# Kernel optimization log

Hardware: AMD Instinct MI355X
Metric: run time of the kernel (lower is better)

The kernel has to match this reference:

```python
import jax, jax.numpy as jnp
import numpy as np

THRESHOLD = 0.0  # default float threshold, non-learned path
SURROGATE_TAU = 0.1

@jax.custom_vjp
def jumprelu(x):
    # Forward: hard threshold x * 1[x > THRESHOLD]
    return x * (x > THRESHOLD).astype(x.dtype)

def _jumprelu_fwd(x):
    return jumprelu(x), x

def _jumprelu_bwd(x, g):
    # Smooth surrogate gradient of x * sigmoid(x/tau)
    tau = SURROGATE_TAU
    sig = jax.nn.sigmoid(x / tau)
    surrogate = sig + x * sig * (1.0 - sig) / tau
    return (g * surrogate,)

jumprelu.defvjp(_jumprelu_fwd, _jumprelu_bwd)

NUM_TRANSFORMS = 64
D_MODEL = 2048
RANK = 32
BATCH = 2048

def setup_inputs() -> dict:
    key = jax.random.key(0)
    kx, kv, ku, ke = jax.random.split(key, 4)
    scale = (1.0 / (D_MODEL * RANK)) ** 0.25
    x = jax.random.normal(kx, (BATCH, D_MODEL), dtype=jnp.float32)
    V = jax.random.normal(kv, (NUM_TRANSFORMS, RANK, D_MODEL), dtype=jnp.float32) * scale
    U = jax.random.normal(ku, (NUM_TRANSFORMS, D_MODEL, RANK), dtype=jnp.float32) * scale
    encoder = jax.random.normal(ke, (NUM_TRANSFORMS, D_MODEL), dtype=jnp.float32)
    encoder = encoder / jnp.linalg.norm(encoder, axis=1, keepdims=True)
    bias = jnp.full((NUM_TRANSFORMS,), -1.0, dtype=jnp.float32)
    return {"x": x, "V": V, "U": U, "encoder": encoder, "bias": bias}

def reference(x, V, U, encoder, bias):
    # pre_acts: (batch, num_transforms)
    pre_acts = x @ encoder.T - bias
    gate = jumprelu(pre_acts)
    # Vx: (n, b, r); UVx: (n, b, d)
    Vx = jnp.einsum('nrd,bd->nbr', V, x)
    UVx = jnp.einsum('ndr,nbr->nbd', U, Vx)
    gated = UVx * gate.T[:, :, None]
    output = gated.sum(axis=0)  # (batch, d_model)
    u_norms = jnp.linalg.norm(U.reshape(U.shape[0], -1), axis=1)
    v_norms = jnp.linalg.norm(V.reshape(V.shape[0], -1), axis=1)
    frobenius_norms = u_norms * v_norms / (D_MODEL * RANK) ** 0.5
    return (output, gate, frobenius_norms)
```

## Files before the change

### kernel.cpp

```cpp
#include <hip/hip_runtime.h>


#define D_MODEL 2048
#define BATCH   2048
#define NT      64
#define RANK    32

typedef __attribute__((ext_vector_type(8))) __bf16 bf16x8;
typedef __attribute__((ext_vector_type(4))) float  f32x4;

__device__ __forceinline__ unsigned short f2bf(float f) {
  unsigned int u = __builtin_bit_cast(unsigned int, f);
  u += 0x7FFFu + ((u >> 16) & 1u);
  return (unsigned short)(u >> 16);
}

__device__ __forceinline__ void gload_lds16(const void* g, void* l) {
  __builtin_amdgcn_global_load_lds(
      (const __attribute__((address_space(1))) unsigned int*)g,
      (__attribute__((address_space(3))) unsigned int*)l,
      16, 0, 0);
}


__device__ __forceinline__ void block_reduce_store(float ss, float* dst, int slot) {
  __shared__ float red[256];
  int t = threadIdx.x;
  red[t] = ss;
  __syncthreads();
  for (int s = 128; s > 0; s >>= 1) {
    if (t < s) red[t] += red[t + s];
    __syncthreads();
  }
  if (t == 0) dst[slot] = red[0];
}

__global__ void k_prep(const float4* __restrict__ x, const float4* __restrict__ enc,
                       const float4* __restrict__ V, const float4* __restrict__ U,
                       ushort4* __restrict__ xb, ushort4* __restrict__ encb,
                       ushort4* __restrict__ Vb, unsigned short* __restrict__ Ut,
                       float* __restrict__ partV, float* __restrict__ partU) {
  int bid = blockIdx.x, t = threadIdx.x;
  if (bid < 1024) {
#pragma unroll
    for (int it = 0; it < 4; ++it) {
      int i = bid * 1024 + it * 256 + t;
      float4 v = x[i];
      ushort4 o;
      o.x = f2bf(v.x); o.y = f2bf(v.y); o.z = f2bf(v.z); o.w = f2bf(v.w);
      xb[i] = o;
    }
  } else if (bid < 1152) {
    int i = (bid - 1024) * 256 + t;
    float4 v = enc[i];
    ushort4 o;
    o.x = f2bf(v.x); o.y = f2bf(v.y); o.z = f2bf(v.z); o.w = f2bf(v.w);
    encb[i] = o;
  } else if (bid < 1408) {
    int b = bid - 1152;
    size_t base4 = (size_t)b * 4096;
    float ss = 0.f;
    for (int it = 0; it < 16; ++it) {
      size_t idx = base4 + t + it * 256;
      float4 v = V[idx];
      ss += v.x * v.x + v.y * v.y + v.z * v.z + v.w * v.w;
      ushort4 o;
      o.x = f2bf(v.x); o.y = f2bf(v.y); o.z = f2bf(v.z); o.w = f2bf(v.w);
      Vb[idx] = o;
    }
    block_reduce_store(ss, partV, b);
  } else {
    int b = bid - 1408;
    int n = b >> 2;
    size_t base4 = (size_t)b * 4096;
    float ss = 0.f;
    for (int it = 0; it < 16; ++it) {
      size_t idx4 = base4 + t + it * 256;
      float4 v = U[idx4];
      ss += v.x * v.x + v.y * v.y + v.z * v.z + v.w * v.w;
      size_t e = idx4 * 4 - (size_t)n * (D_MODEL * RANK);
      int dcol = (int)(e >> 5);
      int r = (int)(e & 31);
      ushort4 o;
      o.x = f2bf(v.x); o.y = f2bf(v.y); o.z = f2bf(v.z); o.w = f2bf(v.w);
      *(ushort4*)(Ut + (size_t)dcol * 2048 + n * 32 + r) = o;
    }
    block_reduce_store(ss, partU, b);
  }
}

__global__ void k_gate_reduce(const float* __restrict__ part, const float* __restrict__ bias,
                              float* __restrict__ gate,
                              const float* __restrict__ pU, const float* __restrict__ pV,
                              float* __restrict__ frob) {
  int t = threadIdx.x;
  if (blockIdx.x == 0 && t < NT) {
    float su = pU[4 * t] + pU[4 * t + 1] + pU[4 * t + 2] + pU[4 * t + 3];
    float sv = pV[4 * t] + pV[4 * t + 1] + pV[4 * t + 2] + pV[4 * t + 3];
    frob[t] = sqrtf(su) * sqrtf(sv) * (1.0f / 256.0f);
  }
#pragma unroll
  for (int u = 0; u < 4; ++u) {
    int idx = blockIdx.x * 1024 + u * 256 + t;
    float s = 0.f;
#pragma unroll
    for (int z = 0; z < 8; ++z) s += part[(size_t)z * (BATCH * NT) + idx];
    float pre = s - bias[idx & (NT - 1)];
    gate[idx] = pre > 0.f ? pre : 0.f;
  }
}

template <int WGM, int WGN, int MI, int NJ, int EPI, int SWZ, int TEAMS>
__global__ __launch_bounds__(TEAMS * 256, 4)
void gemm_bt(const unsigned short* __restrict__ A,
             const unsigned short* __restrict__ Bt,
             const float* __restrict__ aux,
             unsigned short* __restrict__ outB,
             float* __restrict__ outF, int K, int klen) {
  constexpr int BM = WGM * MI * 16;
  constexpr int BN = WGN * NJ * 16;
  constexpr int RA = BM / 32;
  constexpr int RB = BN / 32;
  __shared__ __align__(16) unsigned short smem[TEAMS * (BM + BN) * 64];

  const int tid = threadIdx.x;
  const int w = tid >> 6;
  const int lane = tid & 63;
  const int quad = lane >> 4;
  const int l15 = lane & 15;
  const int team = w >> 2;
  const int wl = w & 3;
  const int wm = wl % WGM;
  const int wn = wl / WGM;

  unsigned short* As = smem + team * (BM + BN) * 64;
  unsigned short* Bs = As + BM * 64;

  int blockM, blockN, kbeg;
  if constexpr (SWZ) {
    const int lin = blockIdx.x;
    const int xcd = lin & 7;
    const int i = lin >> 3;
    blockM = (xcd & 1) * 8 + (i & 7);
    blockN = (xcd >> 1) * 8 + (i >> 3);
    kbeg = 0;
  } else {
    blockN = blockIdx.x;
    blockM = blockIdx.y;
    kbeg = blockIdx.z * klen;
  }
  const int kspan = klen / TEAMS;
  kbeg += team * kspan;

  const int lrow = lane >> 3;
  const int lq = (lane & 7) ^ lrow;
  const unsigned short* Ag = A + (size_t)(blockM * BM + lrow) * K + kbeg + lq * 8;
  const unsigned short* Bg = Bt + (size_t)(blockN * BN + lrow) * K + kbeg + lq * 8;

  const int pcs = (quad ^ (lane & 7)) * 16;
  const int rfA = wm * MI * 16 + l15;
  const int rfB = wn * NJ * 16 + l15;

  f32x4 acc[MI][NJ];
  const f32x4 z = {0.f, 0.f, 0.f, 0.f};
#pragma unroll
  for (int i = 0; i < MI; ++i)
#pragma unroll
    for (int j = 0; j < NJ; ++j) acc[i][j] = z;

  for (int k0 = 0; k0 < kspan; k0 += 64) {
#pragma unroll
    for (int j = 0; j < RA; ++j)
      gload_lds16(Ag + (size_t)((j * 4 + wl) * 8) * K + k0,
                  (char*)As + (j * 4 + wl) * 1024);
#pragma unroll
    for (int j = 0; j < RB; ++j)
      gload_lds16(Bg + (size_t)((j * 4 + wl) * 8) * K + k0,
                  (char*)Bs + (j * 4 + wl) * 1024);
    __syncthreads();
#pragma unroll
    for (int s = 0; s < 2; ++s) {
      bf16x8 af[MI], bfr[NJ];
#pragma unroll
      for (int i = 0; i < MI; ++i)
        af[i] = *(const bf16x8*)((const char*)As + (rfA + i * 16) * 128 + (pcs ^ (s << 6)));
#pragma unroll
      for (int j = 0; j < NJ; ++j)
        bfr[j] = *(const bf16x8*)((const char*)Bs + (rfB + j * 16) * 128 + (pcs ^ (s << 6)));
#pragma unroll
      for (int i = 0; i < MI; ++i)
#pragma unroll
        for (int j = 0; j < NJ; ++j)
          acc[i][j] = __builtin_amdgcn_mfma_f32_16x16x32_bf16(af[i], bfr[j], acc[i][j], 0, 0, 0);
    }
    __syncthreads();
  }

  if constexpr (TEAMS == 2) {
    float4* red = (float4*)smem;
    if (team == 1) {
#pragma unroll
      for (int i = 0; i < MI; ++i)
#pragma unroll
        for (int j = 0; j < NJ; ++j) {
          float4 v = {acc[i][j][0], acc[i][j][1], acc[i][j][2], acc[i][j][3]};
          red[((wl * MI + i) * NJ + j) * 64 + lane] = v;
        }
    }
    __syncthreads();
    if (team == 1) return;
#pragma unroll
    for (int i = 0; i < MI; ++i)
#pragma unroll
      for (int j = 0; j < NJ; ++j) {
        float4 r = red[((wl * MI + i) * NJ + j) * 64 + lane];
        acc[i][j][0] += r.x; acc[i][j][1] += r.y;
        acc[i][j][2] += r.z; acc[i][j][3] += r.w;
      }
  }

  const int row0 = blockM * BM + wm * MI * 16 + quad * 4;
  const int col0 = blockN * BN + wn * NJ * 16 + l15;
#pragma unroll
  for (int i = 0; i < MI; ++i) {
#pragma unroll
    for (int j = 0; j < NJ; ++j) {
      const int col = col0 + j * 16;
#pragma unroll
      for (int t = 0; t < 4; ++t) {
        const int row = row0 + i * 16 + t;
        float v = acc[i][j][t];
        if constexpr (EPI == 0) {
          float g = aux[(size_t)row * NT + (col >> 5)];
          outB[(size_t)row * 2048 + col] = f2bf(v * g);
        } else if constexpr (EPI == 1) {
          outF[(size_t)row * 2048 + col] = v;
        } else {
          outF[(size_t)blockIdx.z * (BATCH * NT) + (size_t)row * NT + col] = v;
        }
      }
    }
  }
}


extern "C" void kernel_launch(void* const* d_in, const int* in_sizes, int n_in,
                              void* d_out, int out_size, void* d_ws, size_t ws_size,
                              hipStream_t stream) {
  const float* x    = (const float*)d_in[0];
  const float* V    = (const float*)d_in[1];
  const float* U    = (const float*)d_in[2];
  const float* enc  = (const float*)d_in[3];
  const float* bias = (const float*)d_in[4];

  float* out  = (float*)d_out;
  float* gate = out + (size_t)BATCH * D_MODEL;
  float* frob = gate + (size_t)BATCH * NT;

  char* ws = (char*)d_ws;
  unsigned short* xb   = (unsigned short*)(ws);
  unsigned short* Vb   = (unsigned short*)(ws + (8u << 20));
  unsigned short* Ut   = (unsigned short*)(ws + (16u << 20));
  unsigned short* Yg   = (unsigned short*)(ws + (24u << 20));
  float* gatePart      = (float*)Yg;
  unsigned short* encb = (unsigned short*)(ws + (32u << 20));
  float* partU = (float*)(ws + (32u << 20) + 262144);
  float* partV = partU + 256;

  k_prep<<<1664, 256, 0, stream>>>((const float4*)x, (const float4*)enc,
                                   (const float4*)V, (const float4*)U,
                                   (ushort4*)xb, (ushort4*)encb, (ushort4*)Vb, Ut,
                                   partV, partU);

  gemm_bt<4, 1, 2, 4, 3, 0, 1><<<dim3(1, 16, 8), 256, 0, stream>>>(
      xb, encb, nullptr, nullptr, gatePart, D_MODEL, 256);
  k_gate_reduce<<<128, 256, 0, stream>>>(gatePart, bias, gate, partU, partV, frob);

  gemm_bt<2, 2, 4, 2, 0, 1, 2><<<dim3(512, 1, 1), 512, 0, stream>>>(
      xb, Vb, gate, Yg, nullptr, D_MODEL, D_MODEL);

  gemm_bt<2, 2, 4, 2, 1, 1, 2><<<dim3(512, 1, 1), 512, 0, stream>>>(
      Yg, Ut, nullptr, nullptr, out, D_MODEL, D_MODEL);
}
```

Before: 154.3 us.

## Double-buffer LDS in GEMM and replace split-K teams with larger tiles

Drops the two-team intra-block split-K reduction from the bf16 GEMM kernel. It now double-buffers the LDS tiles so the next K-slice's global-to-LDS loads overlap the current MFMA work, using one barrier per iteration instead of two. The two big GEMMs now use 8 waves per 128x128 tile (256 blocks instead of 512), with a new XCD-aware block swizzle and launch bounds of 2. The trade is more LDS per block and fewer blocks to hide latency, in exchange for removing the LDS reduction and overlapping loads with compute.

```diff
diff --git a/kernel.cpp b/kernel.cpp
--- a/kernel.cpp
+++ b/kernel.cpp
@@ -110,47 +110,42 @@
   }
 }
 
-template <int WGM, int WGN, int MI, int NJ, int EPI, int SWZ, int TEAMS>
-__global__ __launch_bounds__(TEAMS * 256, 4)
+template <int WGM, int WGN, int MI, int NJ, int EPI, int SWZ>
+__global__ __launch_bounds__(WGM * WGN * 64, 2)
 void gemm_bt(const unsigned short* __restrict__ A,
              const unsigned short* __restrict__ Bt,
              const float* __restrict__ aux,
              unsigned short* __restrict__ outB,
              float* __restrict__ outF, int K, int klen) {
+  constexpr int VW = WGM * WGN;
   constexpr int BM = WGM * MI * 16;
   constexpr int BN = WGN * NJ * 16;
-  constexpr int RA = BM / 32;
-  constexpr int RB = BN / 32;
-  __shared__ __align__(16) unsigned short smem[TEAMS * (BM + BN) * 64];
+  constexpr int GA = (BM / 8) / VW;
+  constexpr int GB = (BN / 8) / VW;
+  constexpr int HBUF = (BM + BN) * 64;
+  __shared__ __align__(16) unsigned short smem[2 * HBUF];
 
   const int tid = threadIdx.x;
   const int w = tid >> 6;
   const int lane = tid & 63;
   const int quad = lane >> 4;
   const int l15 = lane & 15;
-  const int team = w >> 2;
-  const int wl = w & 3;
-  const int wm = wl % WGM;
-  const int wn = wl / WGM;
-
-  unsigned short* As = smem + team * (BM + BN) * 64;
-  unsigned short* Bs = As + BM * 64;
+  const int wm = w % WGM;
+  const int wn = w / WGM;
 
   int blockM, blockN, kbeg;
   if constexpr (SWZ) {
     const int lin = blockIdx.x;
     const int xcd = lin & 7;
     const int i = lin >> 3;
-    blockM = (xcd & 1) * 8 + (i & 7);
-    blockN = (xcd >> 1) * 8 + (i >> 3);
+    blockM = (xcd & 3) * 4 + (i & 3);
+    blockN = (xcd >> 2) * 8 + (i >> 2);
     kbeg = 0;
   } else {
     blockN = blockIdx.x;
     blockM = blockIdx.y;
     kbeg = blockIdx.z * klen;
   }
-  const int kspan = klen / TEAMS;
-  kbeg += team * kspan;
 
   const int lrow = lane >> 3;
   const int lq = (lane & 7) ^ lrow;
@@ -168,16 +163,28 @@
 #pragma unroll
     for (int j = 0; j < NJ; ++j) acc[i][j] = z;
 
-  for (int k0 = 0; k0 < kspan; k0 += 64) {
-#pragma unroll
-    for (int j = 0; j < RA; ++j)
-      gload_lds16(Ag + (size_t)((j * 4 + wl) * 8) * K + k0,
-                  (char*)As + (j * 4 + wl) * 1024);
-#pragma unroll
-    for (int j = 0; j < RB; ++j)
-      gload_lds16(Bg + (size_t)((j * 4 + wl) * 8) * K + k0,
-                  (char*)Bs + (j * 4 + wl) * 1024);
-    __syncthreads();
+  auto stage = [&](int buf, int k0) {
+    unsigned short* As = smem + buf * HBUF;
+    unsigned short* Bs = As + BM * 64;
+#pragma unroll
+    for (int j = 0; j < GA; ++j)
+      gload_lds16(Ag + (size_t)((j * VW + w) * 8) * K + k0,
+                  (char*)As + (j * VW + w) * 1024);
+#pragma unroll
+    for (int j = 0; j < GB; ++j)
+      gload_lds16(Bg + (size_t)((j * VW + w) * 8) * K + k0,
+                  (char*)Bs + (j * VW + w) * 1024);
+  };
+
+  stage(0, 0);
+  __syncthreads();
+
+  const int nt = klen / 64;
+  int cur = 0;
+  for (int t = 0; t < nt; ++t) {
+    if (t + 1 < nt) stage(cur ^ 1, (t + 1) * 64);
+    const unsigned short* As = smem + cur * HBUF;
+    const unsigned short* Bs = As + BM * 64;
 #pragma unroll
     for (int s = 0; s < 2; ++s) {
       bf16x8 af[MI], bfr[NJ];
@@ -194,29 +201,7 @@
           acc[i][j] = __builtin_amdgcn_mfma_f32_16x16x32_bf16(af[i], bfr[j], acc[i][j], 0, 0, 0);
     }
     __syncthreads();
-  }
-
-  if constexpr (TEAMS == 2) {
-    float4* red = (float4*)smem;
-    if (team == 1) {
-#pragma unroll
-      for (int i = 0; i < MI; ++i)
-#pragma unroll
-        for (int j = 0; j < NJ; ++j) {
-          float4 v = {acc[i][j][0], acc[i][j][1], acc[i][j][2], acc[i][j][3]};
-          red[((wl * MI + i) * NJ + j) * 64 + lane] = v;
-        }
-    }
-    __syncthreads();
-    if (team == 1) return;
-#pragma unroll
-    for (int i = 0; i < MI; ++i)
-#pragma unroll
-      for (int j = 0; j < NJ; ++j) {
-        float4 r = red[((wl * MI + i) * NJ + j) * 64 + lane];
-        acc[i][j][0] += r.x; acc[i][j][1] += r.y;
-        acc[i][j][2] += r.z; acc[i][j][3] += r.w;
-      }
+    cur ^= 1;
   }
 
   const int row0 = blockM * BM + wm * MI * 16 + quad * 4;
@@ -272,13 +257,13 @@
                                    (ushort4*)xb, (ushort4*)encb, (ushort4*)Vb, Ut,
                                    partV, partU);
 
-  gemm_bt<4, 1, 2, 4, 3, 0, 1><<<dim3(1, 16, 8), 256, 0, stream>>>(
+  gemm_bt<4, 1, 2, 4, 3, 0><<<dim3(1, 16, 8), 256, 0, stream>>>(
       xb, encb, nullptr, nullptr, gatePart, D_MODEL, 256);
   k_gate_reduce<<<128, 256, 0, stream>>>(gatePart, bias, gate, partU, partV, frob);
 
-  gemm_bt<2, 2, 4, 2, 0, 1, 2><<<dim3(512, 1, 1), 512, 0, stream>>>(
+  gemm_bt<2, 4, 4, 2, 0, 1><<<dim3(256, 1, 1), 512, 0, stream>>>(
       xb, Vb, gate, Yg, nullptr, D_MODEL, D_MODEL);
 
-  gemm_bt<2, 2, 4, 2, 1, 1, 2><<<dim3(512, 1, 1), 512, 0, stream>>>(
+  gemm_bt<2, 4, 4, 2, 1, 1><<<dim3(256, 1, 1), 512, 0, stream>>>(
       Yg, Ut, nullptr, nullptr, out, D_MODEL, D_MODEL);
 }
```

Result: no change. 156.5 us (+1.5%).
